# Kernel tuning notes

Measured on AMD Instinct MI355X. Metric: run time of the kernel, lower is better.

The kernel has to match this reference:

```python
import jax, jax.numpy as jnp
import numpy as np

MODES = 2
N = 6000
KNN = 15
NODES = 512
LC = 3  # number of hidden layers
SCALE = 0.05


def _gen_coo(n, knn):
    # One (row, col) pair per CK_inputs entry: node i couples to 2*(knn+1)
    # neighbors i-knn .. i+knn+1, clipped to valid range. Duplicates at the
    # boundaries are summed on scatter (matches torch sparse coalesce()).
    offsets = np.arange(-knn, knn + 2)            # 2*(knn+1) offsets
    rows = np.repeat(np.arange(n), 2 * (knn + 1))
    cols = np.clip((np.arange(n)[:, None] + offsets[None, :]).reshape(-1), 0, n - 1)
    return rows.astype(np.int32), cols.astype(np.int32)


def setup_inputs() -> dict:
    key = jax.random.key(0)
    k0, k1, k2, k3 = jax.random.split(key, 4)
    CK_inputs = jax.random.normal(k0, (N, 2 * (KNN + 1), 3), dtype=jnp.float32)
    W_in = (jax.random.normal(k1, (3, NODES), dtype=jnp.float32) * SCALE)
    b_in = jnp.zeros((NODES,), dtype=jnp.float32)
    Wh = (jax.random.normal(k2, (LC, NODES, NODES), dtype=jnp.float32) * SCALE)
    bh = jnp.zeros((LC, NODES), dtype=jnp.float32)
    W_out = (jax.random.normal(k3, (NODES, MODES ** 2), dtype=jnp.float32) * SCALE)
    b_out = jnp.zeros((MODES ** 2,), dtype=jnp.float32)
    rows_np, cols_np = _gen_coo(N, KNN)
    return {
        "CK_inputs": CK_inputs,
        "W_in": W_in, "b_in": b_in,
        "Wh": Wh, "bh": bh,
        "W_out": W_out, "b_out": b_out,
        "rows": jnp.asarray(rows_np), "cols": jnp.asarray(cols_np),
    }


def reference(CK_inputs, W_in, b_in, Wh, bh, W_out, b_out, rows, cols):
    n = CK_inputs.shape[0]
    modes = int(np.sqrt(b_out.shape[0]))
    # MLP over all E = N*2*(Knn+1) couplings: [E,3] -> [E, modes^2]
    x = CK_inputs.reshape(-1, 3)
    h = jax.nn.relu(x @ W_in + b_in)
    for l in range(Wh.shape[0]):  # small fixed layer count
        h = jax.nn.relu(h @ Wh[l] + bh[l])
    vals = (h @ W_out + b_out).reshape(-1, modes, modes)  # [E, mi, mj]
    # Fused scatter-add: original builds modes^2 sparse COO tensors with
    # indices (r*modes+mi, c*modes+mj), sums, coalesces, densifies. That is
    # exactly dense[r, mi, c, mj] += vals[e, mi, mj].
    dense = jnp.zeros((n, modes, n, modes), dtype=CK_inputs.dtype)
    dense = dense.at[rows, :, cols, :].add(vals)
    return dense.reshape(n * modes, n * modes)
```

## Files before the change

kernel.cpp:

```cpp
#include <hip/hip_runtime.h>

#define NN     6000
#define KNN    15
#define EPB    32
#define HID    512
#define NLAYER 3
#define OUTDIM 12000
#define MB     96
#define NTH    512
#define NKT    16
#define NG     (NLAYER * NKT)

typedef _Float16 half8  __attribute__((ext_vector_type(8)));
typedef _Float16 half4v __attribute__((ext_vector_type(4)));
typedef float    floatx4 __attribute__((ext_vector_type(4)));

__global__ void prep_weights(const float* __restrict__ Wh, _Float16* __restrict__ Wt)
{
    const int blk = blockIdx.x;
    const int ln  = threadIdx.x;
    const int nt  = blk & 31;
    const int kt  = (blk >> 5) & 15;
    const int l   = blk >> 9;
    const int lc  = ln & 15, lg = ln >> 4;
    const float* src = Wh + (size_t)l * HID * HID
                          + (size_t)(kt * 32 + lg * 8) * HID + nt * 16 + lc;
    half8 v;
#pragma unroll
    for (int j = 0; j < 8; ++j) v[j] = (_Float16)src[(size_t)j * HID];
    *(half8*)(Wt + (size_t)blk * 512 + ln * 8) = v;
}

__global__ __launch_bounds__(NTH, 1)
void mlp_mfma_kernel(const float* __restrict__ CK,
                     const float* __restrict__ W_in,
                     const float* __restrict__ b_in,
                     const float* __restrict__ bh,
                     const float* __restrict__ W_out,
                     const float* __restrict__ b_out,
                     const _Float16* __restrict__ Wt,
                     float* __restrict__ out)
{
    extern __shared__ float4 smem4[];
    _Float16* Ah = (_Float16*)smem4;
    __shared__ float  xs[MB * 3];
    __shared__ float4 edgeval[MB];
    __shared__ float  bandv[3][2][80];

    const int t  = threadIdx.x;
    const int w  = t >> 6;
    const int ln = t & 63;
    const int lc = ln & 15;
    const int lg = ln >> 4;
    const int kbase = lg * 8;
    const int swzA  = (lc & 7) << 3;
    const int m  = blockIdx.x;

    const floatx4 z4 = (floatx4){0.f, 0.f, 0.f, 0.f};
#define ZROW(Q) do {                                                           \
        const int n_   = 3 * m + ((Q) >> 1);                                   \
        const int cmin_ = (n_ - KNN < 0) ? 0 : n_ - KNN;                       \
        const int cmax_ = (n_ + KNN + 1 > NN - 1) ? NN - 1 : n_ + KNN + 1;     \
        const int end_  = 2 * cmin_ + 2 * (cmax_ - cmin_ + 1);                 \
        const int wlo_  = (2 * cmin_) & ~3;                                    \
        const int whi_  = (end_ + 3) & ~3;                                     \
        float* rowp_ = out + (size_t)(6 * m + (Q)) * OUTDIM;                   \
        for (int i_ = t; i_ < OUTDIM / 4; i_ += NTH) {                         \
            const int j_ = 4 * i_;                                             \
            if (j_ < wlo_ || j_ >= whi_)                                       \
                __builtin_nontemporal_store(z4, (floatx4*)(rowp_ + j_));       \
        }                                                                      \
    } while (0)

    const half8* __restrict__ Wt8 = (const half8*)Wt + (size_t)(w * 4) * 64 + ln;

    half8 bA[4], bB[4];
#pragma unroll
    for (int nf = 0; nf < 4; ++nf) bA[nf] = Wt8[(size_t)0 * 2048 + nf * 64];
#pragma unroll
    for (int nf = 0; nf < 4; ++nf) bB[nf] = Wt8[(size_t)1 * 2048 + nf * 64];

    if (t < MB * 3) xs[t] = CK[(size_t)m * (MB * 3) + t];
    __syncthreads();

    {
        const int j0 = t;
        const float wi0 = W_in[j0], wi1 = W_in[HID + j0], wi2 = W_in[2 * HID + j0];
        const float bi  = b_in[j0];
#pragma unroll 8
        for (int r = 0; r < MB; ++r) {
            float a = fmaf(xs[r * 3 + 2], wi2,
                      fmaf(xs[r * 3 + 1], wi1,
                      fmaf(xs[r * 3 + 0], wi0, bi)));
            Ah[r * HID + (j0 ^ ((r & 7) << 3))] = (_Float16)fmaxf(a, 0.f);
        }
    }
    __syncthreads();

#define KSTEP(G, RCUR) do {                                                    \
        half8 a_[6];                                                           \
        const int kb_ = ((G) & 15) * 32 + kbase;                               \
        _Pragma("unroll")                                                      \
        for (int mf_ = 0; mf_ < 6; ++mf_)                                      \
            a_[mf_] = *(const half8*)&Ah[(mf_ * 16 + lc) * HID + (kb_ ^ swzA)];\
        __builtin_amdgcn_s_setprio(1);                                         \
        _Pragma("unroll")                                                      \
        for (int mf_ = 0; mf_ < 6; ++mf_)                                      \
            _Pragma("unroll")                                                  \
            for (int nf_ = 0; nf_ < 4; ++nf_)                                  \
                acc[mf_][nf_] = __builtin_amdgcn_mfma_f32_16x16x32_f16(        \
                    RCUR[nf_], a_[mf_], acc[mf_][nf_], 0, 0, 0);               \
        __builtin_amdgcn_s_setprio(0);                                         \
        if ((G) + 2 < NG) {                                                    \
            _Pragma("unroll")                                                  \
            for (int nf_ = 0; nf_ < 4; ++nf_)                                  \
                RCUR[nf_] = Wt8[(size_t)((G) + 2) * 2048 + nf_ * 64];          \
        }                                                                      \
    } while (0)

    for (int layer = 0; layer < NLAYER; ++layer) {
        const float* __restrict__ bias = bh + layer * HID;

        floatx4 acc[6][4];
#pragma unroll
        for (int nf = 0; nf < 4; ++nf) {
            const floatx4 bv = *(const floatx4*)&bias[w * 64 + nf * 16 + lg * 4];
#pragma unroll
            for (int mf = 0; mf < 6; ++mf) acc[mf][nf] = bv;
        }

        ZROW(layer * 2);
        ZROW(layer * 2 + 1);

#pragma unroll
        for (int kt2 = 0; kt2 < NKT; kt2 += 2) {
            const int g = layer * NKT + kt2;
            KSTEP(g,     bA);
            KSTEP(g + 1, bB);
        }

        __syncthreads();
#pragma unroll
        for (int mf = 0; mf < 6; ++mf) {
            const int r = mf * 16 + lc;
#pragma unroll
            for (int nf = 0; nf < 4; ++nf) {
                const int n0 = w * 64 + nf * 16 + lg * 4;
                half4v h4;
#pragma unroll
                for (int j = 0; j < 4; ++j)
                    h4[j] = (_Float16)fmaxf(acc[mf][nf][j], 0.f);
                *(half4v*)&Ah[r * HID + (n0 ^ swzA)] = h4;
            }
        }
        __syncthreads();
    }

    {
        const int s = t & 7;
        const float4 bo = *(const float4*)b_out;
#pragma unroll
        for (int pass = 0; pass < 2; ++pass) {
            const int rr = pass * 64 + (t >> 3);
            if (rr < MB) {
                const int swzr = (rr & 7) << 3;
                float p0 = 0.f, p1 = 0.f, p2 = 0.f, p3 = 0.f;
                for (int i = 0; i < HID / 8; ++i) {
                    const int k = s + i * 8;
                    const float hv = (float)Ah[rr * HID + (k ^ swzr)];
                    const floatx4 wv = *(const floatx4*)&W_out[k * 4];
                    p0 = fmaf(hv, wv[0], p0);
                    p1 = fmaf(hv, wv[1], p1);
                    p2 = fmaf(hv, wv[2], p2);
                    p3 = fmaf(hv, wv[3], p3);
                }
#pragma unroll
                for (int mm = 1; mm < 8; mm <<= 1) {
                    p0 += __shfl_xor(p0, mm, 64);
                    p1 += __shfl_xor(p1, mm, 64);
                    p2 += __shfl_xor(p2, mm, 64);
                    p3 += __shfl_xor(p3, mm, 64);
                }
                if (s == 0)
                    edgeval[rr] = make_float4(p0 + bo.x, p1 + bo.y,
                                              p2 + bo.z, p3 + bo.w);
            }
        }
    }
    __syncthreads();

    if (t < 96) {
        const int nd = t >> 5, ci = t & 31;
        const int n  = 3 * m + nd;
        const int cmin  = (n - KNN < 0) ? 0 : n - KNN;
        const int cmax  = (n + KNN + 1 > NN - 1) ? NN - 1 : n + KNN + 1;
        const int width = cmax - cmin + 1;
        if (ci < width) {
            const int c = cmin + ci;
            int e_lo, e_hi;
            if (c == 0)           { e_lo = 0;                  e_hi = KNN - n; }
            else if (c == NN - 1) { e_lo = (NN - 1) - n + KNN; e_hi = EPB - 1; }
            else                  { e_lo = e_hi = c - n + KNN; }
            float s0 = 0.f, s1 = 0.f, s2 = 0.f, s3 = 0.f;
            for (int e = e_lo; e <= e_hi; ++e) {
                const float4 pv = edgeval[nd * EPB + e];
                s0 += pv.x; s1 += pv.y; s2 += pv.z; s3 += pv.w;
            }
            bandv[nd][0][2 * ci] = s0; bandv[nd][0][2 * ci + 1] = s1;
            bandv[nd][1][2 * ci] = s2; bandv[nd][1][2 * ci + 1] = s3;
        }
    }
    __syncthreads();

    if (t < 6 * 80) {
        const int q  = t / 80;
        const int jl = t % 80;
        const int nd = q >> 1, mi = q & 1;
        const int n  = 3 * m + nd;
        const int cmin  = (n - KNN < 0) ? 0 : n - KNN;
        const int cmax  = (n + KNN + 1 > NN - 1) ? NN - 1 : n + KNN + 1;
        const int end   = 2 * cmin + 2 * (cmax - cmin + 1);
        const int wlo   = (2 * cmin) & ~3;
        const int whi   = (end + 3) & ~3;
        const int j     = wlo + jl;
        if (j < whi) {
            const bool inside = (j >= 2 * cmin) && (j < end);
            const float v = inside ? bandv[nd][mi][j - 2 * cmin] : 0.f;
            out[(size_t)(6 * m + q) * OUTDIM + j] = v;
        }
    }
}

extern "C" void kernel_launch(void* const* d_in, const int* in_sizes, int n_in,
                              void* d_out, int out_size, void* d_ws, size_t ws_size,
                              hipStream_t stream) {
    const float* CK    = (const float*)d_in[0];
    const float* W_in  = (const float*)d_in[1];
    const float* b_in  = (const float*)d_in[2];
    const float* Wh    = (const float*)d_in[3];
    const float* bh    = (const float*)d_in[4];
    const float* W_out = (const float*)d_in[5];
    const float* b_out = (const float*)d_in[6];
    float* out = (float*)d_out;

    _Float16* Wt = (_Float16*)d_ws;

    (void)ws_size;
    hipFuncSetAttribute((const void*)mlp_mfma_kernel,
                        hipFuncAttributeMaxDynamicSharedMemorySize, 98304);

    prep_weights<<<NLAYER * 16 * 32, 64, 0, stream>>>(Wh, Wt);
    mlp_mfma_kernel<<<NN / 3, NTH, 98304, stream>>>(CK, W_in, b_in, bh,
                                                    W_out, b_out, Wt, out);
}
```

Before: 383.6 us.

## Switch to 32x32x16 MFMA and enlarge row tile to 128 edges per block

Each block now handles 4 nodes (128 edges) instead of 3 (96), and the hidden-layer GEMMs use 32x32x16 f16 MFMA instead of 16x16x32. The weight prepack, LDS A-fragment loads, accumulator layout, bias init and epilogue are all rewritten to match the new fragment layout. The aim is more reuse of each weight fragment per block, fewer weight reloads across the grid, and denser MFMA issue. In exchange each block needs 128KB of LDS, which limits occupancy, and the grid shrinks to 1500 blocks.

```diff
diff --git a/kernel.cpp b/kernel.cpp
--- a/kernel.cpp
+++ b/kernel.cpp
@@ -6,25 +6,27 @@
 #define HID    512
 #define NLAYER 3
 #define OUTDIM 12000
-#define MB     96
+#define MB     128
 #define NTH    512
 #define NKT    16
 #define NG     (NLAYER * NKT)
 
-typedef _Float16 half8  __attribute__((ext_vector_type(8)));
-typedef _Float16 half4v __attribute__((ext_vector_type(4)));
+typedef _Float16 half8   __attribute__((ext_vector_type(8)));
+typedef _Float16 half4v  __attribute__((ext_vector_type(4)));
 typedef float    floatx4 __attribute__((ext_vector_type(4)));
+typedef float    floatx16 __attribute__((ext_vector_type(16)));
 
 __global__ void prep_weights(const float* __restrict__ Wh, _Float16* __restrict__ Wt)
 {
     const int blk = blockIdx.x;
     const int ln  = threadIdx.x;
-    const int nt  = blk & 31;
+    const int nt  = blk & 15;
+    const int ks2 = (blk >> 4) & 1;
     const int kt  = (blk >> 5) & 15;
     const int l   = blk >> 9;
-    const int lc  = ln & 15, lg = ln >> 4;
-    const float* src = Wh + (size_t)l * HID * HID
-                          + (size_t)(kt * 32 + lg * 8) * HID + nt * 16 + lc;
+    const int k0  = kt * 32 + ks2 * 16 + (ln >> 5) * 8;
+    const int n   = nt * 32 + (ln & 31);
+    const float* src = Wh + (size_t)l * HID * HID + (size_t)k0 * HID + n;
     half8 v;
 #pragma unroll
     for (int j = 0; j < 8; ++j) v[j] = (_Float16)src[(size_t)j * HID];
@@ -45,26 +47,25 @@
     _Float16* Ah = (_Float16*)smem4;
     __shared__ float  xs[MB * 3];
     __shared__ float4 edgeval[MB];
-    __shared__ float  bandv[3][2][80];
+    __shared__ float  bandv[4][2][80];
 
     const int t  = threadIdx.x;
     const int w  = t >> 6;
     const int ln = t & 63;
-    const int lc = ln & 15;
-    const int lg = ln >> 4;
-    const int kbase = lg * 8;
-    const int swzA  = (lc & 7) << 3;
+    const int l5 = ln & 31;
+    const int kg = ln >> 5;
+    const int swzA = (ln & 7) << 3;
     const int m  = blockIdx.x;
 
     const floatx4 z4 = (floatx4){0.f, 0.f, 0.f, 0.f};
 #define ZROW(Q) do {                                                           \
-        const int n_   = 3 * m + ((Q) >> 1);                                   \
+        const int n_   = 4 * m + ((Q) >> 1);                                   \
         const int cmin_ = (n_ - KNN < 0) ? 0 : n_ - KNN;                       \
         const int cmax_ = (n_ + KNN + 1 > NN - 1) ? NN - 1 : n_ + KNN + 1;     \
         const int end_  = 2 * cmin_ + 2 * (cmax_ - cmin_ + 1);                 \
         const int wlo_  = (2 * cmin_) & ~3;                                    \
         const int whi_  = (end_ + 3) & ~3;                                     \
-        float* rowp_ = out + (size_t)(6 * m + (Q)) * OUTDIM;                   \
+        float* rowp_ = out + (size_t)(8 * m + (Q)) * OUTDIM;                   \
         for (int i_ = t; i_ < OUTDIM / 4; i_ += NTH) {                         \
             const int j_ = 4 * i_;                                             \
             if (j_ < wlo_ || j_ >= whi_)                                       \
@@ -72,13 +73,17 @@
         }                                                                      \
     } while (0)
 
-    const half8* __restrict__ Wt8 = (const half8*)Wt + (size_t)(w * 4) * 64 + ln;
+    const half8* __restrict__ Wt8 = (const half8*)Wt + ln;
+    const int wb = 2 * w;
 
     half8 bA[4], bB[4];
 #pragma unroll
-    for (int nf = 0; nf < 4; ++nf) bA[nf] = Wt8[(size_t)0 * 2048 + nf * 64];
-#pragma unroll
-    for (int nf = 0; nf < 4; ++nf) bB[nf] = Wt8[(size_t)1 * 2048 + nf * 64];
+    for (int k2 = 0; k2 < 2; ++k2)
+#pragma unroll
+        for (int c = 0; c < 2; ++c) {
+            bA[k2 * 2 + c] = Wt8[(size_t)(0 * 32 + k2 * 16 + wb + c) * 64];
+            bB[k2 * 2 + c] = Wt8[(size_t)(1 * 32 + k2 * 16 + wb + c) * 64];
+        }
 
     if (t < MB * 3) xs[t] = CK[(size_t)m * (MB * 3) + t];
     __syncthreads();
@@ -98,39 +103,51 @@
     __syncthreads();
 
 #define KSTEP(G, RCUR) do {                                                    \
-        half8 a_[6];                                                           \
-        const int kb_ = ((G) & 15) * 32 + kbase;                               \
+        const int kt_ = ((G) & 15) * 32;                                       \
         _Pragma("unroll")                                                      \
-        for (int mf_ = 0; mf_ < 6; ++mf_)                                      \
-            a_[mf_] = *(const half8*)&Ah[(mf_ * 16 + lc) * HID + (kb_ ^ swzA)];\
-        __builtin_amdgcn_s_setprio(1);                                         \
-        _Pragma("unroll")                                                      \
-        for (int mf_ = 0; mf_ < 6; ++mf_)                                      \
+        for (int k2_ = 0; k2_ < 2; ++k2_) {                                    \
+            half8 a_[4];                                                       \
+            const int kb_ = kt_ + k2_ * 16 + kg * 8;                           \
             _Pragma("unroll")                                                  \
-            for (int nf_ = 0; nf_ < 4; ++nf_)                                  \
-                acc[mf_][nf_] = __builtin_amdgcn_mfma_f32_16x16x32_f16(        \
-                    RCUR[nf_], a_[mf_], acc[mf_][nf_], 0, 0, 0);               \
-        __builtin_amdgcn_s_setprio(0);                                         \
+            for (int rf_ = 0; rf_ < 4; ++rf_)                                  \
+                a_[rf_] = *(const half8*)                                      \
+                    &Ah[(rf_ * 32 + l5) * HID + (kb_ ^ swzA)];                 \
+            __builtin_amdgcn_s_setprio(1);                                     \
+            _Pragma("unroll")                                                  \
+            for (int rf_ = 0; rf_ < 4; ++rf_)                                  \
+                _Pragma("unroll")                                              \
+                for (int cf_ = 0; cf_ < 2; ++cf_)                              \
+                    acc[rf_][cf_] = __builtin_amdgcn_mfma_f32_32x32x16_f16(    \
+                        RCUR[k2_ * 2 + cf_], a_[rf_], acc[rf_][cf_], 0, 0, 0); \
+            __builtin_amdgcn_s_setprio(0);                                     \
+        }                                                                      \
         if ((G) + 2 < NG) {                                                    \
             _Pragma("unroll")                                                  \
-            for (int nf_ = 0; nf_ < 4; ++nf_)                                  \
-                RCUR[nf_] = Wt8[(size_t)((G) + 2) * 2048 + nf_ * 64];          \
+            for (int k2_ = 0; k2_ < 2; ++k2_)                                  \
+                _Pragma("unroll")                                              \
+                for (int c_ = 0; c_ < 2; ++c_)                                 \
+                    RCUR[k2_ * 2 + c_] = Wt8[(size_t)(((G) + 2) * 32           \
+                                             + k2_ * 16 + wb + c_) * 64];      \
         }                                                                      \
     } while (0)
 
     for (int layer = 0; layer < NLAYER; ++layer) {
         const float* __restrict__ bias = bh + layer * HID;
 
-        floatx4 acc[6][4];
-#pragma unroll
-        for (int nf = 0; nf < 4; ++nf) {
-            const floatx4 bv = *(const floatx4*)&bias[w * 64 + nf * 16 + lg * 4];
-#pragma unroll
-            for (int mf = 0; mf < 6; ++mf) acc[mf][nf] = bv;
-        }
-
-        ZROW(layer * 2);
-        ZROW(layer * 2 + 1);
+        floatx16 acc[4][2];
+#pragma unroll
+        for (int cf = 0; cf < 2; ++cf) {
+            floatx16 bv;
+#pragma unroll
+            for (int reg = 0; reg < 16; ++reg)
+                bv[reg] = bias[w * 64 + cf * 32 + (reg & 3) + 8 * (reg >> 2) + 4 * kg];
+#pragma unroll
+            for (int rf = 0; rf < 4; ++rf) acc[rf][cf] = bv;
+        }
+
+        ZROW(layer * 3);
+        ZROW(layer * 3 + 1);
+        if (layer < 2) ZROW(layer * 3 + 2);
 
 #pragma unroll
         for (int kt2 = 0; kt2 < NKT; kt2 += 2) {
@@ -141,16 +158,19 @@
 
         __syncthreads();
 #pragma unroll
-        for (int mf = 0; mf < 6; ++mf) {
-            const int r = mf * 16 + lc;
-#pragma unroll
-            for (int nf = 0; nf < 4; ++nf) {
-                const int n0 = w * 64 + nf * 16 + lg * 4;
-                half4v h4;
-#pragma unroll
-                for (int j = 0; j < 4; ++j)
-                    h4[j] = (_Float16)fmaxf(acc[mf][nf][j], 0.f);
-                *(half4v*)&Ah[r * HID + (n0 ^ swzA)] = h4;
+        for (int rf = 0; rf < 4; ++rf) {
+            const int r = rf * 32 + l5;
+#pragma unroll
+            for (int cf = 0; cf < 2; ++cf) {
+#pragma unroll
+                for (int g4 = 0; g4 < 4; ++g4) {
+                    const int ng = w * 64 + cf * 32 + 8 * g4 + 4 * kg;
+                    half4v h4;
+#pragma unroll
+                    for (int i = 0; i < 4; ++i)
+                        h4[i] = (_Float16)fmaxf(acc[rf][cf][g4 * 4 + i], 0.f);
+                    *(half4v*)&Ah[r * HID + (ng ^ swzA)] = h4;
+                }
             }
         }
         __syncthreads();
@@ -162,36 +182,33 @@
 #pragma unroll
         for (int pass = 0; pass < 2; ++pass) {
             const int rr = pass * 64 + (t >> 3);
-            if (rr < MB) {
-                const int swzr = (rr & 7) << 3;
-                float p0 = 0.f, p1 = 0.f, p2 = 0.f, p3 = 0.f;
-                for (int i = 0; i < HID / 8; ++i) {
-                    const int k = s + i * 8;
-                    const float hv = (float)Ah[rr * HID + (k ^ swzr)];
-                    const floatx4 wv = *(const floatx4*)&W_out[k * 4];
-                    p0 = fmaf(hv, wv[0], p0);
-                    p1 = fmaf(hv, wv[1], p1);
-                    p2 = fmaf(hv, wv[2], p2);
-                    p3 = fmaf(hv, wv[3], p3);
-                }
-#pragma unroll
-                for (int mm = 1; mm < 8; mm <<= 1) {
-                    p0 += __shfl_xor(p0, mm, 64);
-                    p1 += __shfl_xor(p1, mm, 64);
-                    p2 += __shfl_xor(p2, mm, 64);
-                    p3 += __shfl_xor(p3, mm, 64);
-                }
-                if (s == 0)
-                    edgeval[rr] = make_float4(p0 + bo.x, p1 + bo.y,
-                                              p2 + bo.z, p3 + bo.w);
-            }
-        }
-    }
-    __syncthreads();
-
-    if (t < 96) {
+            const int swzr = (rr & 7) << 3;
+            float p0 = 0.f, p1 = 0.f, p2 = 0.f, p3 = 0.f;
+            for (int i = 0; i < HID / 8; ++i) {
+                const int k = s + i * 8;
+                const float hv = (float)Ah[rr * HID + (k ^ swzr)];
+                const floatx4 wv = *(const floatx4*)&W_out[k * 4];
+                p0 = fmaf(hv, wv[0], p0);
+                p1 = fmaf(hv, wv[1], p1);
+                p2 = fmaf(hv, wv[2], p2);
+                p3 = fmaf(hv, wv[3], p3);
+            }
+#pragma unroll
+            for (int mm = 1; mm < 8; mm <<= 1) {
+                p0 += __shfl_xor(p0, mm, 64);
+                p1 += __shfl_xor(p1, mm, 64);
+                p2 += __shfl_xor(p2, mm, 64);
+                p3 += __shfl_xor(p3, mm, 64);
+            }
+            if (s == 0)
+                edgeval[rr] = make_float4(p0 + bo.x, p1 + bo.y, p2 + bo.z, p3 + bo.w);
+        }
+    }
+    __syncthreads();
+
+    if (t < 128) {
         const int nd = t >> 5, ci = t & 31;
-        const int n  = 3 * m + nd;
+        const int n  = 4 * m + nd;
         const int cmin  = (n - KNN < 0) ? 0 : n - KNN;
         const int cmax  = (n + KNN + 1 > NN - 1) ? NN - 1 : n + KNN + 1;
         const int width = cmax - cmin + 1;
@@ -212,21 +229,24 @@
     }
     __syncthreads();
 
-    if (t < 6 * 80) {
-        const int q  = t / 80;
-        const int jl = t % 80;
-        const int nd = q >> 1, mi = q & 1;
-        const int n  = 3 * m + nd;
-        const int cmin  = (n - KNN < 0) ? 0 : n - KNN;
-        const int cmax  = (n + KNN + 1 > NN - 1) ? NN - 1 : n + KNN + 1;
-        const int end   = 2 * cmin + 2 * (cmax - cmin + 1);
-        const int wlo   = (2 * cmin) & ~3;
-        const int whi   = (end + 3) & ~3;
-        const int j     = wlo + jl;
-        if (j < whi) {
-            const bool inside = (j >= 2 * cmin) && (j < end);
-            const float v = inside ? bandv[nd][mi][j - 2 * cmin] : 0.f;
-            out[(size_t)(6 * m + q) * OUTDIM + j] = v;
+#pragma unroll
+    for (int pass = 0; pass < 2; ++pass) {
+        if (t < 320) {
+            const int q  = pass * 4 + t / 80;
+            const int jl = t % 80;
+            const int nd = q >> 1, mi = q & 1;
+            const int n  = 4 * m + nd;
+            const int cmin  = (n - KNN < 0) ? 0 : n - KNN;
+            const int cmax  = (n + KNN + 1 > NN - 1) ? NN - 1 : n + KNN + 1;
+            const int end   = 2 * cmin + 2 * (cmax - cmin + 1);
+            const int wlo   = (2 * cmin) & ~3;
+            const int whi   = (end + 3) & ~3;
+            const int j     = wlo + jl;
+            if (j < whi) {
+                const bool inside = (j >= 2 * cmin) && (j < end);
+                const float v = inside ? bandv[nd][mi][j - 2 * cmin] : 0.f;
+                out[(size_t)(8 * m + q) * OUTDIM + j] = v;
+            }
         }
     }
 }
@@ -247,9 +267,9 @@
 
     (void)ws_size;
     hipFuncSetAttribute((const void*)mlp_mfma_kernel,
-                        hipFuncAttributeMaxDynamicSharedMemorySize, 98304);
-
-    prep_weights<<<NLAYER * 16 * 32, 64, 0, stream>>>(Wh, Wt);
-    mlp_mfma_kernel<<<NN / 3, NTH, 98304, stream>>>(CK, W_in, b_in, bh,
-                                                    W_out, b_out, Wt, out);
+                        hipFuncAttributeMaxDynamicSharedMemorySize, 131072);
+
+    prep_weights<<<NLAYER * 16 * 2 * 16, 64, 0, stream>>>(Wh, Wt);
+    mlp_mfma_kernel<<<NN / 4, NTH, 131072, stream>>>(CK, W_in, b_in, bh,
+                                                     W_out, b_out, Wt, out);
 }
```

Measured after the change: 459.2 us. +19.7%, slower.
